# Optimization experiments

Hardware: AMD Instinct MI355X
Metric: run time of the kernel (lower is better)

The kernel has to match this reference:

```python
import jax, jax.numpy as jnp
import numpy as np

B, M, H = 512, 3, 768

def setup_inputs() -> dict:
    key = jax.random.key(0)
    ks = jax.random.split(key, 11)
    s = 1.0 / np.sqrt(H)
    return {
        "target": jax.random.normal(ks[0], (B, H), jnp.float32),
        "cont": jax.random.normal(ks[1], (B, M, H), jnp.float32),
        "Wq": jax.random.uniform(ks[2], (H, H), jnp.float32, -s, s),
        "bq": jax.random.uniform(ks[3], (H,), jnp.float32, -s, s),
        "Wk": jax.random.uniform(ks[4], (H, H), jnp.float32, -s, s),
        "bk": jax.random.uniform(ks[5], (H,), jnp.float32, -s, s),
        "Wv": jax.random.uniform(ks[6], (H, H), jnp.float32, -s, s),
        "bv": jax.random.uniform(ks[7], (H,), jnp.float32, -s, s),
        "p": jax.random.normal(ks[8], (M, H), jnp.float32),
        "h": jax.random.normal(ks[9], (M * H, M), jnp.float32),
        "g": jax.random.normal(ks[10], (M, H), jnp.float32),
    }

def reference(target, cont, Wq, bq, Wk, bk, Wv, bv, p, h, g):
    m = p.shape[0]
    hid = target.shape[-1]
    # torch nn.Linear: y = x @ W.T + b
    query = target @ Wq.T + bq                      # [B, H]
    key_ = cont @ Wk.T + bk                          # [B, m, H]
    value = cont @ Wv.T + bv                         # [B, m, H]
    # kernel_v = p @ query  -> [B, m]
    kernel_v = jnp.einsum('mh,bh->bm', p, query)
    # q = one @ query^T broadcasts query over the m rows, then * key
    x_q = query[:, None, :] * key_                   # [B, m, H]
    kernel_r = x_q.reshape(-1, m * hid) @ h          # [B, m]
    kernel = kernel_v + kernel_r                     # [B, m]
    # _xg = value^T @ g -> [B, H, H]
    _xg = jnp.einsum('bmh,mk->bhk', value, g)        # [B, H, H]
    x_nr = jnp.einsum('bmh,bhk->bmk', value, _xg)    # [B, m, H]
    context = x_nr + value                           # [B, m, H]
    output = jnp.einsum('bm,bmh->bh', kernel, context)  # [B, H]
    return output
```

## Files before the change

kernel.cpp:

```cpp
#include <hip/hip_runtime.h>
#include <hip/hip_bf16.h>

#define HID 768
#define NB  512
#define NM  3

typedef __bf16 bf16x8 __attribute__((ext_vector_type(8)));
typedef float  f32x4  __attribute__((ext_vector_type(4)));

__device__ __forceinline__ unsigned short f2bf(float f) {
    unsigned u = __builtin_bit_cast(unsigned, f);
    u += 0x7FFFu + ((u >> 16) & 1u);
    return (unsigned short)(u >> 16);
}

__global__ __launch_bounds__(256) void qkv_gemm(
    const float* __restrict__ target, const float* __restrict__ cont,
    const float* __restrict__ Wq, const float* __restrict__ bq,
    const float* __restrict__ Wk, const float* __restrict__ bk,
    const float* __restrict__ Wv, const float* __restrict__ bv,
    float* __restrict__ ws)
{
    const int KO = NB * HID;
    const int VO = KO + NB * NM * HID;

    int t = blockIdx.x;
    const float *A, *W, *bias;
    float* C;
    int mtiles;
    if (t < 96)       { A = target; W = Wq; bias = bq; C = ws;      mtiles = 8;  }
    else if (t < 384) { t -= 96;  A = cont; W = Wk; bias = bk; C = ws + KO; mtiles = 24; }
    else              { t -= 384; A = cont; W = Wv; bias = bv; C = ws + VO; mtiles = 24; }
    int tn = t / mtiles, tm = t % mtiles;
    int row0 = tm * 64, col0 = tn * 64;

    __shared__ alignas(16) unsigned short Al[64][40];
    __shared__ alignas(16) unsigned short Bl[64][40];

    int tid  = threadIdx.x;
    int r    = tid >> 2;
    int q4   = tid & 3;
    int lane = tid & 63;
    int w    = tid >> 6;
    int wm   = (w & 1) * 32, wn = (w >> 1) * 32;
    int fm   = lane & 15;
    int kof  = (lane >> 4) * 8;

    f32x4 acc00 = {0.f,0.f,0.f,0.f};
    f32x4 acc01 = acc00, acc10 = acc00, acc11 = acc00;

    const float* Arow = A + (size_t)(row0 + r) * HID + q4 * 8;
    const float* Wrow = W + (size_t)(col0 + r) * HID + q4 * 8;

    for (int k0 = 0; k0 < HID; k0 += 32) {
        float4 a0 = *(const float4*)(Arow + k0);
        float4 a1 = *(const float4*)(Arow + k0 + 4);
        float4 b0 = *(const float4*)(Wrow + k0);
        float4 b1 = *(const float4*)(Wrow + k0 + 4);
        unsigned short ta[8] = { f2bf(a0.x), f2bf(a0.y), f2bf(a0.z), f2bf(a0.w),
                                 f2bf(a1.x), f2bf(a1.y), f2bf(a1.z), f2bf(a1.w) };
        unsigned short tb[8] = { f2bf(b0.x), f2bf(b0.y), f2bf(b0.z), f2bf(b0.w),
                                 f2bf(b1.x), f2bf(b1.y), f2bf(b1.z), f2bf(b1.w) };
        __syncthreads();
        *(uint4*)&Al[r][q4 * 8] = *(uint4*)ta;
        *(uint4*)&Bl[r][q4 * 8] = *(uint4*)tb;
        __syncthreads();

        bf16x8 af0 = *(const bf16x8*)&Al[wm + fm][kof];
        bf16x8 af1 = *(const bf16x8*)&Al[wm + 16 + fm][kof];
        bf16x8 bf0 = *(const bf16x8*)&Bl[wn + fm][kof];
        bf16x8 bf1 = *(const bf16x8*)&Bl[wn + 16 + fm][kof];
        acc00 = __builtin_amdgcn_mfma_f32_16x16x32_bf16(af0, bf0, acc00, 0, 0, 0);
        acc01 = __builtin_amdgcn_mfma_f32_16x16x32_bf16(af0, bf1, acc01, 0, 0, 0);
        acc10 = __builtin_amdgcn_mfma_f32_16x16x32_bf16(af1, bf0, acc10, 0, 0, 0);
        acc11 = __builtin_amdgcn_mfma_f32_16x16x32_bf16(af1, bf1, acc11, 0, 0, 0);
    }

    int crow = row0 + wm + (lane >> 4) * 4;
    int ccol = col0 + wn + fm;
    float bb0 = bias[ccol], bb1 = bias[ccol + 16];
    #pragma unroll
    for (int rg = 0; rg < 4; rg++) {
        C[(size_t)(crow + rg)      * HID + ccol]      = acc00[rg] + bb0;
        C[(size_t)(crow + rg)      * HID + ccol + 16] = acc01[rg] + bb1;
        C[(size_t)(crow + 16 + rg) * HID + ccol]      = acc10[rg] + bb0;
        C[(size_t)(crow + 16 + rg) * HID + ccol + 16] = acc11[rg] + bb1;
    }
}

__global__ __launch_bounds__(256) void finalize(
    const float* __restrict__ ws, const float* __restrict__ p,
    const float* __restrict__ hmat, const float* __restrict__ g,
    float* __restrict__ out)
{
    const int KO = NB * HID;
    const int VO = KO + NB * NM * HID;
    int b    = blockIdx.x;
    int tid  = threadIdx.x;
    int lane = tid & 63;
    int wv   = tid >> 6;

    const float* q  = ws + (size_t)b * HID;
    const float* kk = ws + KO + (size_t)b * NM * HID;
    const float* vv = ws + VO + (size_t)b * NM * HID;

    float acc[12];
    #pragma unroll
    for (int i = 0; i < 12; i++) acc[i] = 0.f;

    for (int h0 = tid; h0 < HID; h0 += 256) {
        float qh = q[h0];
        float k0 = kk[h0], k1 = kk[HID + h0], k2 = kk[2 * HID + h0];
        float v0 = vv[h0], v1 = vv[HID + h0], v2 = vv[2 * HID + h0];
        acc[0] += p[h0] * qh;
        acc[1] += p[HID + h0] * qh;
        acc[2] += p[2 * HID + h0] * qh;
        float x0 = qh * k0, x1 = qh * k1, x2 = qh * k2;
        const float* h0p = hmat + (size_t)h0 * 3;
        const float* h1p = hmat + (size_t)(HID + h0) * 3;
        const float* h2p = hmat + (size_t)(2 * HID + h0) * 3;
        acc[3] += x0 * h0p[0] + x1 * h1p[0] + x2 * h2p[0];
        acc[4] += x0 * h0p[1] + x1 * h1p[1] + x2 * h2p[1];
        acc[5] += x0 * h0p[2] + x1 * h1p[2] + x2 * h2p[2];
        acc[6]  += v0 * v0; acc[7]  += v0 * v1; acc[8]  += v0 * v2;
        acc[9]  += v1 * v1; acc[10] += v1 * v2; acc[11] += v2 * v2;
    }

    #pragma unroll
    for (int i = 0; i < 12; i++)
        #pragma unroll
        for (int off = 32; off > 0; off >>= 1)
            acc[i] += __shfl_down(acc[i], off);

    __shared__ float sred[12][4];
    __shared__ float fin[12];
    if (lane == 0) {
        #pragma unroll
        for (int i = 0; i < 12; i++) sred[i][wv] = acc[i];
    }
    __syncthreads();
    if (tid < 12) fin[tid] = sred[tid][0] + sred[tid][1] + sred[tid][2] + sred[tid][3];
    __syncthreads();

    float kern0 = fin[0] + fin[3], kern1 = fin[1] + fin[4], kern2 = fin[2] + fin[5];
    float S00 = fin[6], S01 = fin[7], S02 = fin[8];
    float S11 = fin[9], S12 = fin[10], S22 = fin[11];

    for (int c = tid; c < HID; c += 256) {
        float g0 = g[c], g1 = g[HID + c], g2 = g[2 * HID + c];
        float v0 = vv[c], v1 = vv[HID + c], v2 = vv[2 * HID + c];
        float c0 = S00 * g0 + S01 * g1 + S02 * g2 + v0;
        float c1 = S01 * g0 + S11 * g1 + S12 * g2 + v1;
        float c2 = S02 * g0 + S12 * g1 + S22 * g2 + v2;
        out[(size_t)b * HID + c] = kern0 * c0 + kern1 * c1 + kern2 * c2;
    }
}

extern "C" void kernel_launch(void* const* d_in, const int* in_sizes, int n_in,
                              void* d_out, int out_size, void* d_ws, size_t ws_size,
                              hipStream_t stream) {
    (void)in_sizes; (void)n_in; (void)out_size; (void)ws_size;
    const float* target = (const float*)d_in[0];
    const float* cont   = (const float*)d_in[1];
    const float* Wq     = (const float*)d_in[2];
    const float* bq     = (const float*)d_in[3];
    const float* Wk     = (const float*)d_in[4];
    const float* bk     = (const float*)d_in[5];
    const float* Wv     = (const float*)d_in[6];
    const float* bv     = (const float*)d_in[7];
    const float* p      = (const float*)d_in[8];
    const float* hmat   = (const float*)d_in[9];
    const float* g      = (const float*)d_in[10];
    float* ws  = (float*)d_ws;
    float* out = (float*)d_out;

    qkv_gemm<<<672, 256, 0, stream>>>(target, cont, Wq, bq, Wk, bk, Wv, bv, ws);
    finalize<<<512, 256, 0, stream>>>(ws, p, hmat, g, out);
}
```

Measured before the change: 112.5 us.

## Pre-convert inputs and weights to bf16 and load GEMM tiles via async global-to-LDS

Adds a separate conversion kernel that writes bf16 copies of target, cont and the three weight matrices into the workspace. The GEMM then streams these bf16 tiles straight into LDS with global_load_lds instead of loading fp32 and converting in registers. This halves the bytes each GEMM tile reads and removes per-iteration conversion ALU work, at the cost of an extra kernel launch and a full fp32 read plus bf16 write pass. The LDS padding is removed, which may bring back bank conflicts on the fragment reads.

New measurement: 102.7 us. 1.09x faster.

```diff
diff --git a/kernel.cpp b/kernel.cpp
--- a/kernel.cpp
+++ b/kernel.cpp
@@ -7,6 +7,11 @@
 
 typedef __bf16 bf16x8 __attribute__((ext_vector_type(8)));
 typedef float  f32x4  __attribute__((ext_vector_type(4)));
+
+#define WBF_OFF   1572864
+#define QKV_OFF   1671168
+#define QN        393216
+#define KVN       1179648
 
 __device__ __forceinline__ unsigned short f2bf(float f) {
     unsigned u = __builtin_bit_cast(unsigned, f);
@@ -14,56 +19,80 @@
     return (unsigned short)(u >> 16);
 }
 
+__device__ __forceinline__ void async_cp16(const void* g, void* l) {
+    __builtin_amdgcn_global_load_lds(
+        (const __attribute__((address_space(1))) void*)g,
+        (__attribute__((address_space(3))) void*)l, 16, 0, 0);
+}
+
+__global__ __launch_bounds__(256) void cvt(
+    const float4* __restrict__ t, const float4* __restrict__ c,
+    const float4* __restrict__ wq, const float4* __restrict__ wk,
+    const float4* __restrict__ wv, ushort4* __restrict__ abf,
+    ushort4* __restrict__ wbf)
+{
+    int i = blockIdx.x * 256 + threadIdx.x;
+    float4 v;
+    ushort4* d;
+    if (i < 393216) {
+        v = (i < 98304) ? t[i] : c[i - 98304];
+        d = abf + i;
+    } else {
+        int j = i - 393216;
+        v = (j < 147456) ? wq[j] : (j < 294912 ? wk[j - 147456] : wv[j - 294912]);
+        d = wbf + j;
+    }
+    ushort4 o = { f2bf(v.x), f2bf(v.y), f2bf(v.z), f2bf(v.w) };
+    *d = o;
+}
+
 __global__ __launch_bounds__(256) void qkv_gemm(
-    const float* __restrict__ target, const float* __restrict__ cont,
-    const float* __restrict__ Wq, const float* __restrict__ bq,
-    const float* __restrict__ Wk, const float* __restrict__ bk,
-    const float* __restrict__ Wv, const float* __restrict__ bv,
-    float* __restrict__ ws)
+    const unsigned short* __restrict__ bf, float* __restrict__ wsf,
+    const float* __restrict__ bq, const float* __restrict__ bk,
+    const float* __restrict__ bv)
 {
-    const int KO = NB * HID;
-    const int VO = KO + NB * NM * HID;
+    const unsigned short* Ab = bf;
+    const unsigned short* Wb = bf + WBF_OFF;
+    float* Qf = wsf + QKV_OFF;
+    float* Kf = Qf + QN;
+    float* Vf = Kf + KVN;
 
     int t = blockIdx.x;
-    const float *A, *W, *bias;
+    const unsigned short *A, *W;
+    const float* bias;
     float* C;
     int mtiles;
-    if (t < 96)       { A = target; W = Wq; bias = bq; C = ws;      mtiles = 8;  }
-    else if (t < 384) { t -= 96;  A = cont; W = Wk; bias = bk; C = ws + KO; mtiles = 24; }
-    else              { t -= 384; A = cont; W = Wv; bias = bv; C = ws + VO; mtiles = 24; }
+    if (t < 96)       {          A = Ab;             W = Wb;              bias = bq; C = Qf; mtiles = 8;  }
+    else if (t < 384) { t -= 96; A = Ab + 512 * HID; W = Wb + 768 * HID;  bias = bk; C = Kf; mtiles = 24; }
+    else              { t -= 384; A = Ab + 512 * HID; W = Wb + 1536 * HID; bias = bv; C = Vf; mtiles = 24; }
     int tn = t / mtiles, tm = t % mtiles;
     int row0 = tm * 64, col0 = tn * 64;
 
-    __shared__ alignas(16) unsigned short Al[64][40];
-    __shared__ alignas(16) unsigned short Bl[64][40];
+    __shared__ unsigned short Al[64][32];
+    __shared__ unsigned short Bl[64][32];
 
     int tid  = threadIdx.x;
-    int r    = tid >> 2;
-    int q4   = tid & 3;
-    int lane = tid & 63;
+    int l    = tid & 63;
     int w    = tid >> 6;
-    int wm   = (w & 1) * 32, wn = (w >> 1) * 32;
-    int fm   = lane & 15;
-    int kof  = (lane >> 4) * 8;
-
-    f32x4 acc00 = {0.f,0.f,0.f,0.f};
+    int srow = tid >> 2;
+    int scol = (tid & 3) * 8;
+
+    const unsigned short* ga = A + (size_t)(row0 + srow) * HID + scol;
+    const unsigned short* gb = W + (size_t)(col0 + srow) * HID + scol;
+    char* la = (char*)&Al[0][0] + w * 1024;
+    char* lb = (char*)&Bl[0][0] + w * 1024;
+
+    int wm = (w & 1) * 32, wn = (w >> 1) * 32;
+    int fm = l & 15, kof = (l >> 4) * 8;
+
+    f32x4 acc00 = {0.f, 0.f, 0.f, 0.f};
     f32x4 acc01 = acc00, acc10 = acc00, acc11 = acc00;
 
-    const float* Arow = A + (size_t)(row0 + r) * HID + q4 * 8;
-    const float* Wrow = W + (size_t)(col0 + r) * HID + q4 * 8;
-
     for (int k0 = 0; k0 < HID; k0 += 32) {
-        float4 a0 = *(const float4*)(Arow + k0);
-        float4 a1 = *(const float4*)(Arow + k0 + 4);
-        float4 b0 = *(const float4*)(Wrow + k0);
-        float4 b1 = *(const float4*)(Wrow + k0 + 4);
-        unsigned short ta[8] = { f2bf(a0.x), f2bf(a0.y), f2bf(a0.z), f2bf(a0.w),
-                                 f2bf(a1.x), f2bf(a1.y), f2bf(a1.z), f2bf(a1.w) };
-        unsigned short tb[8] = { f2bf(b0.x), f2bf(b0.y), f2bf(b0.z), f2bf(b0.w),
-                                 f2bf(b1.x), f2bf(b1.y), f2bf(b1.z), f2bf(b1.w) };
         __syncthreads();
-        *(uint4*)&Al[r][q4 * 8] = *(uint4*)ta;
-        *(uint4*)&Bl[r][q4 * 8] = *(uint4*)tb;
+        async_cp16(ga, la);
+        async_cp16(gb, lb);
+        ga += 32; gb += 32;
         __syncthreads();
 
         bf16x8 af0 = *(const bf16x8*)&Al[wm + fm][kof];
@@ -76,7 +105,7 @@
         acc11 = __builtin_amdgcn_mfma_f32_16x16x32_bf16(af1, bf1, acc11, 0, 0, 0);
     }
 
-    int crow = row0 + wm + (lane >> 4) * 4;
+    int crow = row0 + wm + (l >> 4) * 4;
     int ccol = col0 + wn + fm;
     float bb0 = bias[ccol], bb1 = bias[ccol + 16];
     #pragma unroll
@@ -89,20 +118,18 @@
 }
 
 __global__ __launch_bounds__(256) void finalize(
-    const float* __restrict__ ws, const float* __restrict__ p,
+    const float* __restrict__ wsf, const float* __restrict__ p,
     const float* __restrict__ hmat, const float* __restrict__ g,
     float* __restrict__ out)
 {
-    const int KO = NB * HID;
-    const int VO = KO + NB * NM * HID;
     int b    = blockIdx.x;
     int tid  = threadIdx.x;
     int lane = tid & 63;
     int wv   = tid >> 6;
 
-    const float* q  = ws + (size_t)b * HID;
-    const float* kk = ws + KO + (size_t)b * NM * HID;
-    const float* vv = ws + VO + (size_t)b * NM * HID;
+    const float* q  = wsf + QKV_OFF + (size_t)b * HID;
+    const float* kk = wsf + QKV_OFF + QN + (size_t)b * NM * HID;
+    const float* vv = kk + KVN;
 
     float acc[12];
     #pragma unroll
@@ -171,9 +198,14 @@
     const float* p      = (const float*)d_in[8];
     const float* hmat   = (const float*)d_in[9];
     const float* g      = (const float*)d_in[10];
-    float* ws  = (float*)d_ws;
+
+    unsigned short* bfreg = (unsigned short*)d_ws;
+    float* wsf = (float*)d_ws;
     float* out = (float*)d_out;
 
-    qkv_gemm<<<672, 256, 0, stream>>>(target, cont, Wq, bq, Wk, bk, Wv, bv, ws);
-    finalize<<<512, 256, 0, stream>>>(ws, p, hmat, g, out);
-}
+    cvt<<<3264, 256, 0, stream>>>((const float4*)target, (const float4*)cont,
+                                  (const float4*)Wq, (const float4*)Wk, (const float4*)Wv,
+                                  (ushort4*)bfreg, (ushort4*)(bfreg + WBF_OFF));
+    qkv_gemm<<<672, 256, 0, stream>>>(bfreg, wsf, bq, bk, bv);
+    finalize<<<512, 256, 0, stream>>>(wsf, p, hmat, g, out);
+}
```
